# Kernel optimization log

Hardware: AMD Instinct MI355X
Metric: run time of the kernel (lower is better)

The kernel has to match this reference:

```python
import jax, jax.numpy as jnp
import numpy as np

N_NODES = 50000
IN_C = 128
OUT_C = 128
N_EDGES = 1600000
NEG_SLOPE = 0.2
EPS = 1e-16  # matches torch_geometric softmax denominator epsilon


def setup_inputs() -> dict:
    key = jax.random.key(0)
    k1, k2, k3, k4, k5 = jax.random.split(key, 5)
    glorot = 1.0 / np.sqrt(IN_C)
    x = jax.random.normal(k1, (N_NODES, IN_C), dtype=jnp.float32)
    W = jax.random.normal(k2, (IN_C, OUT_C), dtype=jnp.float32) * glorot
    a_src = jax.random.normal(k3, (OUT_C,), dtype=jnp.float32) * glorot
    a_dst = jax.random.normal(k4, (OUT_C,), dtype=jnp.float32) * glorot
    bias = jnp.zeros((OUT_C,), dtype=jnp.float32)
    edge_index = jax.random.randint(k5, (2, N_EDGES), 0, N_NODES, dtype=jnp.int32)
    return {"x": x, "W": W, "a_src": a_src, "a_dst": a_dst,
            "bias": bias, "edge_index": edge_index}


def reference(x, W, a_src, a_dst, bias, edge_index):
    N = x.shape[0]
    # add self loops (GATConv default add_self_loops=True)
    loops = jnp.arange(N, dtype=edge_index.dtype)
    src = jnp.concatenate([edge_index[0], loops])  # [E+N]
    dst = jnp.concatenate([edge_index[1], loops])

    h = x @ W                                      # [N, out]
    alpha_s = h @ a_src                            # [N]
    alpha_d = h @ a_dst                            # [N]

    e = alpha_s[src] + alpha_d[dst]                # [E+N]
    e = jnp.where(e > 0, e, NEG_SLOPE * e)         # leaky_relu

    # neighbor-wise (per destination node) stable softmax
    m = jax.ops.segment_max(e, dst, num_segments=N)
    ex = jnp.exp(e - m[dst])
    denom = jax.ops.segment_sum(ex, dst, num_segments=N)
    alpha = ex / (denom[dst] + EPS)

    # weighted aggregation of source features into destination nodes
    msgs = h[src] * alpha[:, None]                 # [E+N, out]
    out = jax.ops.segment_sum(msgs, dst, num_segments=N) + bias
    return jax.nn.relu(out)
```

## Files before the change

kernel.cpp:

```cpp
#include <hip/hip_runtime.h>
#include <hip/hip_fp16.h>

#define C 128
#define NEG_SLOPE 0.2f
#define SM_EPS 1e-16f
#define BKT_SHIFT 8
#define BKT_MASK 255
#define BIN_CHUNK 8192
#define WP 136

typedef unsigned int uint32;
typedef __attribute__((ext_vector_type(8))) short bf16x8;
typedef __attribute__((ext_vector_type(4))) float f32x4;

static __device__ __forceinline__ unsigned short f2bf(float f) {
    uint32 u = __float_as_uint(f);
    uint32 r = 0x7FFFu + ((u >> 16) & 1u);
    return (unsigned short)((u + r) >> 16);
}
static __device__ __forceinline__ uint32 f2bf2(float lo, float hi) {
    return (uint32)f2bf(lo) | ((uint32)f2bf(hi) << 16);
}
static __device__ __forceinline__ uint32 f2h(float f) {
    __half h = __float2half(f);
    return (uint32)*reinterpret_cast<unsigned short*>(&h);
}
static __device__ __forceinline__ float h2f(uint32 b) {
    unsigned short s = (unsigned short)(b & 0xffffu);
    __half h = *reinterpret_cast<__half*>(&s);
    return __half2float(h);
}

__global__ __launch_bounds__(256) void cvtw_kernel(const float* __restrict__ W,
                                                   uint32* __restrict__ Wf,
                                                   int* __restrict__ bucket_cnt, int NB) {
    int gid = blockIdx.x * 256 + threadIdx.x;
    if (blockIdx.x == 0 && threadIdx.x < NB) bucket_cnt[threadIdx.x] = 0;
    int j2   = gid & 3;
    int lane = (gid >> 2) & 63;
    int tile = gid >> 8;
    int t = tile >> 2, kk = tile & 3;
    int n = t * 16 + (lane & 15);
    int k = kk * 32 + (lane >> 4) * 8 + j2 * 2;
    Wf[gid] = f2bf2(W[k * C + n], W[(k + 1) * C + n]);
}

__global__ __launch_bounds__(256) void gemm_hist_kernel(
    const float* __restrict__ x, const uint32* __restrict__ Wf,
    const float* __restrict__ a_src, const float* __restrict__ a_dst,
    unsigned short* __restrict__ hb, float* __restrict__ as_out,
    float* __restrict__ ad_out, int N,
    const int* __restrict__ dst, int* __restrict__ bucket_cnt, int E, int total, int NB)
{
    __shared__ __align__(16) unsigned short slice[4][16 * WP];
    __shared__ int bhist[256];

    const int tid  = threadIdx.x;
    const int lane = tid & 63;
    const int w    = tid >> 6;
    const int row0 = blockIdx.x * 64;
    const int m16  = lane & 15;
    const int q    = lane >> 4;

    bhist[tid] = 0;

    const int row = row0 + w * 16 + m16;
    const bool rv = (row < N);
    const float* xr_p = x + (size_t)(rv ? row : 0) * C + q * 8;

    float4 xr[8];
    #pragma unroll
    for (int kk = 0; kk < 4; ++kk) {
        xr[kk * 2]     = rv ? *(const float4*)(xr_p + kk * 32)     : make_float4(0, 0, 0, 0);
        xr[kk * 2 + 1] = rv ? *(const float4*)(xr_p + kk * 32 + 4) : make_float4(0, 0, 0, 0);
    }

    f32x4 acc[8];
    const f32x4 zz = {0.f, 0.f, 0.f, 0.f};
    #pragma unroll
    for (int t = 0; t < 8; ++t) acc[t] = zz;

    #pragma unroll
    for (int kk = 0; kk < 4; ++kk) {
        union { bf16x8 v; uint32 u[4]; } au;
        float4 p0 = xr[kk * 2], p1 = xr[kk * 2 + 1];
        au.u[0] = f2bf2(p0.x, p0.y); au.u[1] = f2bf2(p0.z, p0.w);
        au.u[2] = f2bf2(p1.x, p1.y); au.u[3] = f2bf2(p1.z, p1.w);
        #pragma unroll
        for (int t = 0; t < 8; ++t) {
            bf16x8 b = *(const bf16x8*)&Wf[((t * 4 + kk) * 64 + lane) * 4];
            acc[t] = __builtin_amdgcn_mfma_f32_16x16x32_bf16(au.v, b, acc[t], 0, 0, 0);
        }
    }

    float ps[4] = {0.f, 0.f, 0.f, 0.f}, pd[4] = {0.f, 0.f, 0.f, 0.f};
    #pragma unroll
    for (int t = 0; t < 8; ++t) {
        float av = a_src[t * 16 + m16];
        float dv = a_dst[t * 16 + m16];
        #pragma unroll
        for (int r = 0; r < 4; ++r) {
            ps[r] += acc[t][r] * av;
            pd[r] += acc[t][r] * dv;
        }
    }
    #pragma unroll
    for (int r = 0; r < 4; ++r) {
        #pragma unroll
        for (int off = 1; off < 16; off <<= 1) {
            ps[r] += __shfl_xor(ps[r], off, 64);
            pd[r] += __shfl_xor(pd[r], off, 64);
        }
    }
    if (m16 == 0) {
        #pragma unroll
        for (int r = 0; r < 4; ++r) {
            int rr = row0 + w * 16 + q * 4 + r;
            if (rr < N) { as_out[rr] = ps[r]; ad_out[rr] = pd[r]; }
        }
    }

    #pragma unroll
    for (int t = 0; t < 8; ++t)
        #pragma unroll
        for (int r = 0; r < 4; ++r)
            slice[w][(q * 4 + r) * WP + t * 16 + m16] = f2bf(acc[t][r]);
    __syncthreads();
    #pragma unroll
    for (int it = 0; it < 4; ++it) {
        int r = it * 4 + q;
        int rr = row0 + w * 16 + r;
        if (rr < N) {
            bf16x8 v = *(const bf16x8*)&slice[w][r * WP + m16 * 8];
            *(bf16x8*)&hb[(size_t)rr * C + m16 * 8] = v;
        }
    }

    for (int i = blockIdx.x * 256 + tid; i < total; i += gridDim.x * 256) {
        int d = (i < E) ? dst[i] : (i - E);
        atomicAdd(&bhist[d >> BKT_SHIFT], 1);
    }
    __syncthreads();
    if (tid < NB && bhist[tid]) atomicAdd(&bucket_cnt[tid], bhist[tid]);
}

__global__ __launch_bounds__(256) void scan_off_kernel(
    const int* __restrict__ bucket_cnt, int* __restrict__ bucket_off,
    int* __restrict__ bucket_cursor, int* __restrict__ row_start,
    int NB, int N, int total)
{
    __shared__ int wave_tot[4];
    const int tid = threadIdx.x, lane = tid & 63, wid = tid >> 6;
    int v = (tid < NB) ? bucket_cnt[tid] : 0;
    int x = v;
    #pragma unroll
    for (int off = 1; off < 64; off <<= 1) {
        int t = __shfl_up(x, off, 64);
        if (lane >= off) x += t;
    }
    if (lane == 63) wave_tot[wid] = x;
    __syncthreads();
    int wbase = 0;
    #pragma unroll
    for (int w = 0; w < 4; ++w) wbase += (w < wid) ? wave_tot[w] : 0;
    int excl = wbase + x - v;
    if (tid < NB) { bucket_off[tid] = excl; bucket_cursor[tid] = excl; }
    if (tid == 0) { bucket_off[NB] = total; row_start[N] = total; }
}

__global__ __launch_bounds__(1024) void bin_kernel(
    const int* __restrict__ src, const int* __restrict__ dst,
    int* __restrict__ bucket_cursor, uint32* __restrict__ packed,
    int E, int total, int NB)
{
    __shared__ uint32 lsrc[BIN_CHUNK];
    __shared__ unsigned short ldst[BIN_CHUNK];
    __shared__ int hist[256];
    __shared__ int base[256];
    const int tid = threadIdx.x;
    const int start = blockIdx.x * BIN_CHUNK;
    const int end = min(start + BIN_CHUNK, total);
    const int n = end - start;

    if (tid < 256) hist[tid] = 0;
    for (int i = start + tid; i < end; i += 1024) {
        int s = (i < E) ? src[i] : (i - E);
        int d = (i < E) ? dst[i] : (i - E);
        lsrc[i - start] = (uint32)s;
        ldst[i - start] = (unsigned short)d;
    }
    __syncthreads();
    for (int j = tid; j < n; j += 1024)
        atomicAdd(&hist[ldst[j] >> BKT_SHIFT], 1);
    __syncthreads();
    if (tid < NB) {
        int c = hist[tid];
        base[tid] = c ? atomicAdd(&bucket_cursor[tid], c) : 0;
    }
    if (tid < 256) hist[tid] = 0;
    __syncthreads();
    for (int j = tid; j < n; j += 1024) {
        int d = ldst[j];
        int b = d >> BKT_SHIFT;
        int pos = base[b] + atomicAdd(&hist[b], 1);
        packed[pos] = (lsrc[j] << BKT_SHIFT) | (uint32)(d & BKT_MASK);
    }
}

__global__ __launch_bounds__(1024) void build_kernel(
    const uint32* __restrict__ packed, const int* __restrict__ bucket_off,
    const float* __restrict__ as, const float* __restrict__ ad,
    int* __restrict__ row_start, uint32* __restrict__ csr, int N)
{
    __shared__ int cnt[256];
    __shared__ int cur[256];
    __shared__ float adl[256];
    __shared__ int wave_tot[4];
    const int tid = threadIdx.x;
    const int b = blockIdx.x;
    const int off = bucket_off[b];
    const int end = bucket_off[b + 1];

    if (tid < 256) {
        cnt[tid] = 0;
        int g = (b << BKT_SHIFT) + tid;
        adl[tid] = (g < N) ? ad[g] : 0.f;
    }
    __syncthreads();
    for (int j = off + tid; j < end; j += 1024)
        atomicAdd(&cnt[packed[j] & BKT_MASK], 1);
    __syncthreads();

    int v = 0, x = 0;
    if (tid < 256) {
        const int lane = tid & 63;
        v = cnt[tid]; x = v;
        #pragma unroll
        for (int o = 1; o < 64; o <<= 1) {
            int t = __shfl_up(x, o, 64);
            if (lane >= o) x += t;
        }
        if (lane == 63) wave_tot[tid >> 6] = x;
    }
    __syncthreads();
    if (tid < 256) {
        const int wid = tid >> 6;
        int wbase = 0;
        #pragma unroll
        for (int w = 0; w < 4; ++w) wbase += (w < wid) ? wave_tot[w] : 0;
        int excl = wbase + x - v;
        int g = (b << BKT_SHIFT) + tid;
        if (g < N) row_start[g] = off + excl;
        cur[tid] = excl;
    }
    __syncthreads();

    for (int j = off + tid; j < end; j += 1024) {
        uint32 p = packed[j];
        int l = (int)(p & BKT_MASK);
        int s = (int)(p >> BKT_SHIFT);
        float e = as[s] + adl[l];
        e = (e > 0.f) ? e : NEG_SLOPE * e;
        int pos = atomicAdd(&cur[l], 1);
        csr[off + pos] = ((uint32)s << 16) | f2h(e);
    }
}

__global__ __launch_bounds__(256) void gather_kernel(
    const uint32* __restrict__ csr, const int* __restrict__ row_start,
    const unsigned short* __restrict__ hb, const float* __restrict__ bias,
    float* __restrict__ out, int N)
{
    const int w    = threadIdx.x >> 6;
    const int lane = threadIdx.x & 63;
    const int d = blockIdx.x * 4 + w;
    if (d >= N) return;

    const int beg = row_start[d];
    const int deg = row_start[d + 1] - beg;
    const int c2 = lane << 1;
    float a0 = 0.f, a1 = 0.f;

    if (deg <= 64) {
        uint32 ent = (lane < deg) ? csr[beg + lane] : 0xFC00u;
        float e = h2f(ent);
        float m = e;
        #pragma unroll
        for (int off = 32; off > 0; off >>= 1) m = fmaxf(m, __shfl_xor(m, off, 64));
        float p = (lane < deg) ? __expf(e - m) : 0.f;
        float ssum = p;
        #pragma unroll
        for (int off = 32; off > 0; off >>= 1) ssum += __shfl_xor(ssum, off, 64);
        float wgt = p * (1.f / (ssum + SM_EPS));
        uint32 bc = (ent & 0xffff0000u) | f2h(wgt);

        int t = 0;
        for (; t + 8 <= deg; t += 8) {
            uint32 b0 = (uint32)__shfl((int)bc, t, 64),     b1 = (uint32)__shfl((int)bc, t + 1, 64);
            uint32 b2 = (uint32)__shfl((int)bc, t + 2, 64), b3 = (uint32)__shfl((int)bc, t + 3, 64);
            uint32 b4 = (uint32)__shfl((int)bc, t + 4, 64), b5 = (uint32)__shfl((int)bc, t + 5, 64);
            uint32 b6 = (uint32)__shfl((int)bc, t + 6, 64), b7 = (uint32)__shfl((int)bc, t + 7, 64);
            uint32 u0 = *(const uint32*)&hb[(size_t)(b0 >> 16) * C + c2];
            uint32 u1 = *(const uint32*)&hb[(size_t)(b1 >> 16) * C + c2];
            uint32 u2 = *(const uint32*)&hb[(size_t)(b2 >> 16) * C + c2];
            uint32 u3 = *(const uint32*)&hb[(size_t)(b3 >> 16) * C + c2];
            uint32 u4 = *(const uint32*)&hb[(size_t)(b4 >> 16) * C + c2];
            uint32 u5 = *(const uint32*)&hb[(size_t)(b5 >> 16) * C + c2];
            uint32 u6 = *(const uint32*)&hb[(size_t)(b6 >> 16) * C + c2];
            uint32 u7 = *(const uint32*)&hb[(size_t)(b7 >> 16) * C + c2];
            float w0 = h2f(b0), w1 = h2f(b1), w2 = h2f(b2), w3 = h2f(b3);
            float w4 = h2f(b4), w5 = h2f(b5), w6 = h2f(b6), w7 = h2f(b7);
            a0 += __uint_as_float(u0 << 16) * w0 + __uint_as_float(u1 << 16) * w1
                + __uint_as_float(u2 << 16) * w2 + __uint_as_float(u3 << 16) * w3
                + __uint_as_float(u4 << 16) * w4 + __uint_as_float(u5 << 16) * w5
                + __uint_as_float(u6 << 16) * w6 + __uint_as_float(u7 << 16) * w7;
            a1 += __uint_as_float(u0 & 0xffff0000u) * w0 + __uint_as_float(u1 & 0xffff0000u) * w1
                + __uint_as_float(u2 & 0xffff0000u) * w2 + __uint_as_float(u3 & 0xffff0000u) * w3
                + __uint_as_float(u4 & 0xffff0000u) * w4 + __uint_as_float(u5 & 0xffff0000u) * w5
                + __uint_as_float(u6 & 0xffff0000u) * w6 + __uint_as_float(u7 & 0xffff0000u) * w7;
        }
        for (; t < deg; ++t) {
            uint32 b0 = (uint32)__shfl((int)bc, t, 64);
            uint32 u0 = *(const uint32*)&hb[(size_t)(b0 >> 16) * C + c2];
            float w0 = h2f(b0);
            a0 += __uint_as_float(u0 << 16) * w0;
            a1 += __uint_as_float(u0 & 0xffff0000u) * w0;
        }
    } else if (deg <= 128) {
        uint32 ea = (lane < deg) ? csr[beg + lane] : 0xFC00u;
        uint32 eb = (64 + lane < deg) ? csr[beg + 64 + lane] : 0xFC00u;
        float e0 = h2f(ea), e1 = h2f(eb);
        float m = fmaxf(e0, e1);
        #pragma unroll
        for (int off = 32; off > 0; off >>= 1) m = fmaxf(m, __shfl_xor(m, off, 64));
        float p0 = (lane < deg) ? __expf(e0 - m) : 0.f;
        float p1 = (64 + lane < deg) ? __expf(e1 - m) : 0.f;
        float ssum = p0 + p1;
        #pragma unroll
        for (int off = 32; off > 0; off >>= 1) ssum += __shfl_xor(ssum, off, 64);
        float inv = 1.f / (ssum + SM_EPS);
        uint32 ba = (ea & 0xffff0000u) | f2h(p0 * inv);
        uint32 bb = (eb & 0xffff0000u) | f2h(p1 * inv);
        for (int t = 0; t < deg; ++t) {
            uint32 b0 = (t < 64) ? (uint32)__shfl((int)ba, t, 64)
                                 : (uint32)__shfl((int)bb, t - 64, 64);
            uint32 u0 = *(const uint32*)&hb[(size_t)(b0 >> 16) * C + c2];
            float w0 = h2f(b0);
            a0 += __uint_as_float(u0 << 16) * w0;
            a1 += __uint_as_float(u0 & 0xffff0000u) * w0;
        }
    } else {
        float m = -INFINITY;
        for (int t = lane; t < deg; t += 64)
            m = fmaxf(m, h2f(csr[beg + t]));
        #pragma unroll
        for (int off = 32; off > 0; off >>= 1) m = fmaxf(m, __shfl_xor(m, off, 64));
        float ssum = 0.f;
        for (int t = lane; t < deg; t += 64)
            ssum += __expf(h2f(csr[beg + t]) - m);
        #pragma unroll
        for (int off = 32; off > 0; off >>= 1) ssum += __shfl_xor(ssum, off, 64);
        float inv = 1.f / (ssum + SM_EPS);
        for (int t0 = 0; t0 < deg; t0 += 64) {
            int nc = min(64, deg - t0);
            uint32 ent = (lane < nc) ? csr[beg + t0 + lane] : 0xFC00u;
            float wl = (lane < nc) ? __expf(h2f(ent) - m) * inv : 0.f;
            uint32 bc = (ent & 0xffff0000u) | f2h(wl);
            for (int t = 0; t < nc; ++t) {
                uint32 b0 = (uint32)__shfl((int)bc, t, 64);
                uint32 u0 = *(const uint32*)&hb[(size_t)(b0 >> 16) * C + c2];
                float w0 = h2f(b0);
                a0 += __uint_as_float(u0 << 16) * w0;
                a1 += __uint_as_float(u0 & 0xffff0000u) * w0;
            }
        }
    }

    float2 b2 = *(const float2*)&bias[c2];
    a0 = fmaxf(a0 + b2.x, 0.f);
    a1 = fmaxf(a1 + b2.y, 0.f);
    *(float2*)&out[(size_t)d * C + c2] = make_float2(a0, a1);
}

extern "C" void kernel_launch(void* const* d_in, const int* in_sizes, int n_in,
                              void* d_out, int out_size, void* d_ws, size_t ws_size,
                              hipStream_t stream) {
    const float* x     = (const float*)d_in[0];
    const float* W     = (const float*)d_in[1];
    const float* a_src = (const float*)d_in[2];
    const float* a_dst = (const float*)d_in[3];
    const float* bias  = (const float*)d_in[4];
    const int*   edge  = (const int*)d_in[5];

    const int N = in_sizes[0] / C;
    const int E = in_sizes[5] / 2;
    const int total = E + N;
    const int* src = edge;
    const int* dst = edge + E;
    float* out = (float*)d_out;

    const int NB = (N + BKT_MASK) >> BKT_SHIFT;

    float* ws = (float*)d_ws;
    unsigned short* hb = (unsigned short*)ws;
    float* as = (float*)(hb + (size_t)N * C);
    float* ad = as + N;
    int* row_start     = (int*)(ad + N);
    uint32* packed     = (uint32*)(row_start + (N + 2));
    uint32* csr        = packed + total;
    uint32* Wf         = csr + total;
    int* bucket_cnt    = (int*)(Wf + 8192);
    int* bucket_off    = bucket_cnt + NB;
    int* bucket_cursor = bucket_off + (NB + 1);

    cvtw_kernel<<<32, 256, 0, stream>>>(W, Wf, bucket_cnt, NB);
    gemm_hist_kernel<<<(N + 63) / 64, 256, 0, stream>>>(
        x, Wf, a_src, a_dst, hb, as, ad, N, dst, bucket_cnt, E, total, NB);
    scan_off_kernel<<<1, 256, 0, stream>>>(bucket_cnt, bucket_off, bucket_cursor,
                                           row_start, NB, N, total);
    bin_kernel<<<(total + BIN_CHUNK - 1) / BIN_CHUNK, 1024, 0, stream>>>(
        src, dst, bucket_cursor, packed, E, total, NB);
    build_kernel<<<NB, 1024, 0, stream>>>(packed, bucket_off, as, ad, row_start, csr, N);
    gather_kernel<<<(N + 3) / 4, 256, 0, stream>>>(csr, row_start, hb, bias, out, N);
}
```

Baseline: 206.8 us.

## Process two nodes per wave in gather and fold bucket scan into consumers

The gather kernel now assigns each half-wave to one destination node, with each lane loading four bf16 channels as a uint2 instead of two. This is meant to halve the number of waves and issue wider gather loads. The padded loop runs to the larger of the two degrees, so work is wasted when they differ, and high-degree nodes fall back to a full-wave path. The separate single-block scan launch is removed: bin and build kernels recompute the bucket prefix sum per block, using a progress counter in place of a cursor.

```diff
diff --git a/kernel.cpp b/kernel.cpp
--- a/kernel.cpp
+++ b/kernel.cpp
@@ -33,9 +33,13 @@
 
 __global__ __launch_bounds__(256) void cvtw_kernel(const float* __restrict__ W,
                                                    uint32* __restrict__ Wf,
-                                                   int* __restrict__ bucket_cnt, int NB) {
+                                                   int* __restrict__ bucket_cnt,
+                                                   int* __restrict__ bucket_progress, int NB) {
     int gid = blockIdx.x * 256 + threadIdx.x;
-    if (blockIdx.x == 0 && threadIdx.x < NB) bucket_cnt[threadIdx.x] = 0;
+    if (blockIdx.x == 0 && threadIdx.x < NB) {
+        bucket_cnt[threadIdx.x] = 0;
+        bucket_progress[threadIdx.x] = 0;
+    }
     int j2   = gid & 3;
     int lane = (gid >> 2) & 63;
     int tile = gid >> 8;
@@ -144,45 +148,35 @@
     if (tid < NB && bhist[tid]) atomicAdd(&bucket_cnt[tid], bhist[tid]);
 }
 
-__global__ __launch_bounds__(256) void scan_off_kernel(
-    const int* __restrict__ bucket_cnt, int* __restrict__ bucket_off,
-    int* __restrict__ bucket_cursor, int* __restrict__ row_start,
-    int NB, int N, int total)
-{
-    __shared__ int wave_tot[4];
-    const int tid = threadIdx.x, lane = tid & 63, wid = tid >> 6;
-    int v = (tid < NB) ? bucket_cnt[tid] : 0;
-    int x = v;
-    #pragma unroll
-    for (int off = 1; off < 64; off <<= 1) {
-        int t = __shfl_up(x, off, 64);
-        if (lane >= off) x += t;
-    }
-    if (lane == 63) wave_tot[wid] = x;
-    __syncthreads();
-    int wbase = 0;
-    #pragma unroll
-    for (int w = 0; w < 4; ++w) wbase += (w < wid) ? wave_tot[w] : 0;
-    int excl = wbase + x - v;
-    if (tid < NB) { bucket_off[tid] = excl; bucket_cursor[tid] = excl; }
-    if (tid == 0) { bucket_off[NB] = total; row_start[N] = total; }
-}
-
 __global__ __launch_bounds__(1024) void bin_kernel(
     const int* __restrict__ src, const int* __restrict__ dst,
-    int* __restrict__ bucket_cursor, uint32* __restrict__ packed,
-    int E, int total, int NB)
+    const int* __restrict__ bucket_cnt, int* __restrict__ bucket_progress,
+    uint32* __restrict__ packed, int E, int total, int NB)
 {
     __shared__ uint32 lsrc[BIN_CHUNK];
     __shared__ unsigned short ldst[BIN_CHUNK];
     __shared__ int hist[256];
     __shared__ int base[256];
+    __shared__ int boff[256];
+    __shared__ int wave_tot[4];
     const int tid = threadIdx.x;
     const int start = blockIdx.x * BIN_CHUNK;
     const int end = min(start + BIN_CHUNK, total);
     const int n = end - start;
 
-    if (tid < 256) hist[tid] = 0;
+    int v = 0, xx = 0;
+    if (tid < 256) {
+        hist[tid] = 0;
+        const int lane = tid & 63;
+        v = (tid < NB) ? bucket_cnt[tid] : 0;
+        xx = v;
+        #pragma unroll
+        for (int o = 1; o < 64; o <<= 1) {
+            int t = __shfl_up(xx, o, 64);
+            if (lane >= o) xx += t;
+        }
+        if (lane == 63) wave_tot[tid >> 6] = xx;
+    }
     for (int i = start + tid; i < end; i += 1024) {
         int s = (i < E) ? src[i] : (i - E);
         int d = (i < E) ? dst[i] : (i - E);
@@ -190,12 +184,20 @@
         ldst[i - start] = (unsigned short)d;
     }
     __syncthreads();
+    if (tid < 256) {
+        const int wid = tid >> 6;
+        int wbase = 0;
+        #pragma unroll
+        for (int w = 0; w < 4; ++w) wbase += (w < wid) ? wave_tot[w] : 0;
+        boff[tid] = wbase + xx - v;
+    }
+    __syncthreads();
     for (int j = tid; j < n; j += 1024)
         atomicAdd(&hist[ldst[j] >> BKT_SHIFT], 1);
     __syncthreads();
     if (tid < NB) {
         int c = hist[tid];
-        base[tid] = c ? atomicAdd(&bucket_cursor[tid], c) : 0;
+        base[tid] = boff[tid] + (c ? atomicAdd(&bucket_progress[tid], c) : 0);
     }
     if (tid < 256) hist[tid] = 0;
     __syncthreads();
@@ -208,47 +210,68 @@
 }
 
 __global__ __launch_bounds__(1024) void build_kernel(
-    const uint32* __restrict__ packed, const int* __restrict__ bucket_off,
+    const uint32* __restrict__ packed, const int* __restrict__ bucket_cnt,
     const float* __restrict__ as, const float* __restrict__ ad,
-    int* __restrict__ row_start, uint32* __restrict__ csr, int N)
+    int* __restrict__ row_start, uint32* __restrict__ csr, int N, int NB, int total)
 {
     __shared__ int cnt[256];
     __shared__ int cur[256];
     __shared__ float adl[256];
-    __shared__ int wave_tot[4];
+    __shared__ int boff[256];
+    __shared__ int wave_tot[8];
     const int tid = threadIdx.x;
     const int b = blockIdx.x;
-    const int off = bucket_off[b];
-    const int end = bucket_off[b + 1];
-
-    if (tid < 256) {
+
+    int v = 0, xx = 0;
+    if (tid < 256) {
+        const int lane = tid & 63;
+        v = (tid < NB) ? bucket_cnt[tid] : 0;
+        xx = v;
+        #pragma unroll
+        for (int o = 1; o < 64; o <<= 1) {
+            int t = __shfl_up(xx, o, 64);
+            if (lane >= o) xx += t;
+        }
+        if (lane == 63) wave_tot[tid >> 6] = xx;
         cnt[tid] = 0;
         int g = (b << BKT_SHIFT) + tid;
         adl[tid] = (g < N) ? ad[g] : 0.f;
     }
     __syncthreads();
+    if (tid < 256) {
+        const int wid = tid >> 6;
+        int wbase = 0;
+        #pragma unroll
+        for (int w = 0; w < 4; ++w) wbase += (w < wid) ? wave_tot[w] : 0;
+        boff[tid] = wbase + xx - v;
+    }
+    __syncthreads();
+    const int off = boff[b];
+    const int end = off + ((b < NB) ? bucket_cnt[b] : 0);
+    if (b == 0 && tid == 0) row_start[N] = total;
+
     for (int j = off + tid; j < end; j += 1024)
         atomicAdd(&cnt[packed[j] & BKT_MASK], 1);
     __syncthreads();
 
-    int v = 0, x = 0;
+    int v2 = 0, x2 = 0;
     if (tid < 256) {
         const int lane = tid & 63;
-        v = cnt[tid]; x = v;
+        v2 = cnt[tid]; x2 = v2;
         #pragma unroll
         for (int o = 1; o < 64; o <<= 1) {
-            int t = __shfl_up(x, o, 64);
-            if (lane >= o) x += t;
-        }
-        if (lane == 63) wave_tot[tid >> 6] = x;
+            int t = __shfl_up(x2, o, 64);
+            if (lane >= o) x2 += t;
+        }
+        if (lane == 63) wave_tot[4 + (tid >> 6)] = x2;
     }
     __syncthreads();
     if (tid < 256) {
         const int wid = tid >> 6;
         int wbase = 0;
         #pragma unroll
-        for (int w = 0; w < 4; ++w) wbase += (w < wid) ? wave_tot[w] : 0;
-        int excl = wbase + x - v;
+        for (int w = 0; w < 4; ++w) wbase += (w < wid) ? wave_tot[4 + w] : 0;
+        int excl = wbase + x2 - v2;
         int g = (b << BKT_SHIFT) + tid;
         if (g < N) row_start[g] = off + excl;
         cur[tid] = excl;
@@ -266,6 +289,43 @@
     }
 }
 
+static __device__ __forceinline__ void gather_node_fw(
+    int d, const uint32* __restrict__ csr, const int* __restrict__ row_start,
+    const unsigned short* __restrict__ hb, const float* __restrict__ bias,
+    float* __restrict__ out, int lane)
+{
+    const int beg = row_start[d];
+    const int deg = row_start[d + 1] - beg;
+    const int c2 = lane << 1;
+    float a0 = 0.f, a1 = 0.f;
+    float m = -INFINITY;
+    for (int t = lane; t < deg; t += 64) m = fmaxf(m, h2f(csr[beg + t]));
+    #pragma unroll
+    for (int off = 32; off > 0; off >>= 1) m = fmaxf(m, __shfl_xor(m, off, 64));
+    float ssum = 0.f;
+    for (int t = lane; t < deg; t += 64) ssum += __expf(h2f(csr[beg + t]) - m);
+    #pragma unroll
+    for (int off = 32; off > 0; off >>= 1) ssum += __shfl_xor(ssum, off, 64);
+    float inv = 1.f / (ssum + SM_EPS);
+    for (int t0 = 0; t0 < deg; t0 += 64) {
+        int nc = min(64, deg - t0);
+        uint32 ent = (lane < nc) ? csr[beg + t0 + lane] : 0xFC00u;
+        float wl = (lane < nc) ? __expf(h2f(ent) - m) * inv : 0.f;
+        uint32 bc = (ent & 0xffff0000u) | f2h(wl);
+        for (int t = 0; t < nc; ++t) {
+            uint32 b0 = (uint32)__shfl((int)bc, t, 64);
+            uint32 u0 = *(const uint32*)&hb[(size_t)(b0 >> 16) * C + c2];
+            float w0 = h2f(b0);
+            a0 += __uint_as_float(u0 << 16) * w0;
+            a1 += __uint_as_float(u0 & 0xffff0000u) * w0;
+        }
+    }
+    float2 b2 = *(const float2*)&bias[c2];
+    a0 = fmaxf(a0 + b2.x, 0.f);
+    a1 = fmaxf(a1 + b2.y, 0.f);
+    *(float2*)&out[(size_t)d * C + c2] = make_float2(a0, a1);
+}
+
 __global__ __launch_bounds__(256) void gather_kernel(
     const uint32* __restrict__ csr, const int* __restrict__ row_start,
     const unsigned short* __restrict__ hb, const float* __restrict__ bias,
@@ -273,113 +333,98 @@
 {
     const int w    = threadIdx.x >> 6;
     const int lane = threadIdx.x & 63;
-    const int d = blockIdx.x * 4 + w;
-    if (d >= N) return;
-
-    const int beg = row_start[d];
-    const int deg = row_start[d + 1] - beg;
-    const int c2 = lane << 1;
-    float a0 = 0.f, a1 = 0.f;
-
-    if (deg <= 64) {
-        uint32 ent = (lane < deg) ? csr[beg + lane] : 0xFC00u;
-        float e = h2f(ent);
-        float m = e;
-        #pragma unroll
-        for (int off = 32; off > 0; off >>= 1) m = fmaxf(m, __shfl_xor(m, off, 64));
-        float p = (lane < deg) ? __expf(e - m) : 0.f;
-        float ssum = p;
-        #pragma unroll
-        for (int off = 32; off > 0; off >>= 1) ssum += __shfl_xor(ssum, off, 64);
-        float wgt = p * (1.f / (ssum + SM_EPS));
-        uint32 bc = (ent & 0xffff0000u) | f2h(wgt);
-
-        int t = 0;
-        for (; t + 8 <= deg; t += 8) {
-            uint32 b0 = (uint32)__shfl((int)bc, t, 64),     b1 = (uint32)__shfl((int)bc, t + 1, 64);
-            uint32 b2 = (uint32)__shfl((int)bc, t + 2, 64), b3 = (uint32)__shfl((int)bc, t + 3, 64);
-            uint32 b4 = (uint32)__shfl((int)bc, t + 4, 64), b5 = (uint32)__shfl((int)bc, t + 5, 64);
-            uint32 b6 = (uint32)__shfl((int)bc, t + 6, 64), b7 = (uint32)__shfl((int)bc, t + 7, 64);
-            uint32 u0 = *(const uint32*)&hb[(size_t)(b0 >> 16) * C + c2];
-            uint32 u1 = *(const uint32*)&hb[(size_t)(b1 >> 16) * C + c2];
-            uint32 u2 = *(const uint32*)&hb[(size_t)(b2 >> 16) * C + c2];
-            uint32 u3 = *(const uint32*)&hb[(size_t)(b3 >> 16) * C + c2];
-            uint32 u4 = *(const uint32*)&hb[(size_t)(b4 >> 16) * C + c2];
-            uint32 u5 = *(const uint32*)&hb[(size_t)(b5 >> 16) * C + c2];
-            uint32 u6 = *(const uint32*)&hb[(size_t)(b6 >> 16) * C + c2];
-            uint32 u7 = *(const uint32*)&hb[(size_t)(b7 >> 16) * C + c2];
-            float w0 = h2f(b0), w1 = h2f(b1), w2 = h2f(b2), w3 = h2f(b3);
-            float w4 = h2f(b4), w5 = h2f(b5), w6 = h2f(b6), w7 = h2f(b7);
-            a0 += __uint_as_float(u0 << 16) * w0 + __uint_as_float(u1 << 16) * w1
-                + __uint_as_float(u2 << 16) * w2 + __uint_as_float(u3 << 16) * w3
-                + __uint_as_float(u4 << 16) * w4 + __uint_as_float(u5 << 16) * w5
-                + __uint_as_float(u6 << 16) * w6 + __uint_as_float(u7 << 16) * w7;
-            a1 += __uint_as_float(u0 & 0xffff0000u) * w0 + __uint_as_float(u1 & 0xffff0000u) * w1
-                + __uint_as_float(u2 & 0xffff0000u) * w2 + __uint_as_float(u3 & 0xffff0000u) * w3
-                + __uint_as_float(u4 & 0xffff0000u) * w4 + __uint_as_float(u5 & 0xffff0000u) * w5
-                + __uint_as_float(u6 & 0xffff0000u) * w6 + __uint_as_float(u7 & 0xffff0000u) * w7;
-        }
-        for (; t < deg; ++t) {
-            uint32 b0 = (uint32)__shfl((int)bc, t, 64);
-            uint32 u0 = *(const uint32*)&hb[(size_t)(b0 >> 16) * C + c2];
-            float w0 = h2f(b0);
-            a0 += __uint_as_float(u0 << 16) * w0;
-            a1 += __uint_as_float(u0 & 0xffff0000u) * w0;
-        }
-    } else if (deg <= 128) {
-        uint32 ea = (lane < deg) ? csr[beg + lane] : 0xFC00u;
-        uint32 eb = (64 + lane < deg) ? csr[beg + 64 + lane] : 0xFC00u;
-        float e0 = h2f(ea), e1 = h2f(eb);
-        float m = fmaxf(e0, e1);
-        #pragma unroll
-        for (int off = 32; off > 0; off >>= 1) m = fmaxf(m, __shfl_xor(m, off, 64));
-        float p0 = (lane < deg) ? __expf(e0 - m) : 0.f;
-        float p1 = (64 + lane < deg) ? __expf(e1 - m) : 0.f;
-        float ssum = p0 + p1;
-        #pragma unroll
-        for (int off = 32; off > 0; off >>= 1) ssum += __shfl_xor(ssum, off, 64);
-        float inv = 1.f / (ssum + SM_EPS);
-        uint32 ba = (ea & 0xffff0000u) | f2h(p0 * inv);
-        uint32 bb = (eb & 0xffff0000u) | f2h(p1 * inv);
-        for (int t = 0; t < deg; ++t) {
-            uint32 b0 = (t < 64) ? (uint32)__shfl((int)ba, t, 64)
-                                 : (uint32)__shfl((int)bb, t - 64, 64);
-            uint32 u0 = *(const uint32*)&hb[(size_t)(b0 >> 16) * C + c2];
-            float w0 = h2f(b0);
-            a0 += __uint_as_float(u0 << 16) * w0;
-            a1 += __uint_as_float(u0 & 0xffff0000u) * w0;
-        }
-    } else {
-        float m = -INFINITY;
-        for (int t = lane; t < deg; t += 64)
-            m = fmaxf(m, h2f(csr[beg + t]));
-        #pragma unroll
-        for (int off = 32; off > 0; off >>= 1) m = fmaxf(m, __shfl_xor(m, off, 64));
-        float ssum = 0.f;
-        for (int t = lane; t < deg; t += 64)
-            ssum += __expf(h2f(csr[beg + t]) - m);
-        #pragma unroll
-        for (int off = 32; off > 0; off >>= 1) ssum += __shfl_xor(ssum, off, 64);
-        float inv = 1.f / (ssum + SM_EPS);
-        for (int t0 = 0; t0 < deg; t0 += 64) {
-            int nc = min(64, deg - t0);
-            uint32 ent = (lane < nc) ? csr[beg + t0 + lane] : 0xFC00u;
-            float wl = (lane < nc) ? __expf(h2f(ent) - m) * inv : 0.f;
-            uint32 bc = (ent & 0xffff0000u) | f2h(wl);
-            for (int t = 0; t < nc; ++t) {
-                uint32 b0 = (uint32)__shfl((int)bc, t, 64);
-                uint32 u0 = *(const uint32*)&hb[(size_t)(b0 >> 16) * C + c2];
-                float w0 = h2f(b0);
-                a0 += __uint_as_float(u0 << 16) * w0;
-                a1 += __uint_as_float(u0 & 0xffff0000u) * w0;
-            }
-        }
-    }
-
-    float2 b2 = *(const float2*)&bias[c2];
-    a0 = fmaxf(a0 + b2.x, 0.f);
-    a1 = fmaxf(a1 + b2.y, 0.f);
-    *(float2*)&out[(size_t)d * C + c2] = make_float2(a0, a1);
+    const int half = lane >> 5;
+    const int hl   = lane & 31;
+    const int pair = blockIdx.x * 4 + w;
+    const int d0 = pair * 2;
+    if (d0 >= N) return;
+    const int d = d0 + half;
+    const bool valid = (d < N);
+
+    int beg = 0, deg = 0;
+    if (valid) { beg = row_start[d]; deg = row_start[d + 1] - beg; }
+
+    int wdeg = deg;
+    #pragma unroll
+    for (int off = 32; off > 0; off >>= 1) wdeg = max(wdeg, __shfl_xor(wdeg, off, 64));
+
+    if (wdeg > 64) {
+        gather_node_fw(d0, csr, row_start, hb, bias, out, lane);
+        if (d0 + 1 < N) gather_node_fw(d0 + 1, csr, row_start, hb, bias, out, lane);
+        return;
+    }
+
+    uint32 ent0 = (hl < deg) ? csr[beg + hl] : 0xFC00u;
+    uint32 ent1 = (32 + hl < deg) ? csr[beg + 32 + hl] : 0xFC00u;
+    float e0 = h2f(ent0), e1 = h2f(ent1);
+    float m = fmaxf(e0, e1);
+    #pragma unroll
+    for (int off = 16; off > 0; off >>= 1) m = fmaxf(m, __shfl_xor(m, off, 64));
+    float p0 = (hl < deg) ? __expf(e0 - m) : 0.f;
+    float p1 = (32 + hl < deg) ? __expf(e1 - m) : 0.f;
+    float ssum = p0 + p1;
+    #pragma unroll
+    for (int off = 16; off > 0; off >>= 1) ssum += __shfl_xor(ssum, off, 64);
+    const float inv = 1.f / (ssum + SM_EPS);
+    uint32 bc0 = (hl < deg) ? ((ent0 & 0xffff0000u) | f2h(p0 * inv)) : 0u;
+    uint32 bc1 = (32 + hl < deg) ? ((ent1 & 0xffff0000u) | f2h(p1 * inv)) : 0u;
+
+    const int c4 = hl << 2;
+    const int hbase = half << 5;
+    float a0 = 0.f, a1 = 0.f, a2 = 0.f, a3 = 0.f;
+
+    const int n1 = min(wdeg, 32);
+    int t = 0;
+    for (; t + 2 <= n1; t += 2) {
+        uint32 bA = (uint32)__shfl((int)bc0, hbase + t, 64);
+        uint32 bB = (uint32)__shfl((int)bc0, hbase + t + 1, 64);
+        uint2 uA = *(const uint2*)&hb[(size_t)(bA >> 16) * C + c4];
+        uint2 uB = *(const uint2*)&hb[(size_t)(bB >> 16) * C + c4];
+        float wA = h2f(bA), wB = h2f(bB);
+        a0 += __uint_as_float(uA.x << 16) * wA + __uint_as_float(uB.x << 16) * wB;
+        a1 += __uint_as_float(uA.x & 0xffff0000u) * wA + __uint_as_float(uB.x & 0xffff0000u) * wB;
+        a2 += __uint_as_float(uA.y << 16) * wA + __uint_as_float(uB.y << 16) * wB;
+        a3 += __uint_as_float(uA.y & 0xffff0000u) * wA + __uint_as_float(uB.y & 0xffff0000u) * wB;
+    }
+    for (; t < n1; ++t) {
+        uint32 bA = (uint32)__shfl((int)bc0, hbase + t, 64);
+        uint2 uA = *(const uint2*)&hb[(size_t)(bA >> 16) * C + c4];
+        float wA = h2f(bA);
+        a0 += __uint_as_float(uA.x << 16) * wA;
+        a1 += __uint_as_float(uA.x & 0xffff0000u) * wA;
+        a2 += __uint_as_float(uA.y << 16) * wA;
+        a3 += __uint_as_float(uA.y & 0xffff0000u) * wA;
+    }
+    for (t = 32; t + 2 <= wdeg; t += 2) {
+        uint32 bA = (uint32)__shfl((int)bc1, hbase + t - 32, 64);
+        uint32 bB = (uint32)__shfl((int)bc1, hbase + t - 31, 64);
+        uint2 uA = *(const uint2*)&hb[(size_t)(bA >> 16) * C + c4];
+        uint2 uB = *(const uint2*)&hb[(size_t)(bB >> 16) * C + c4];
+        float wA = h2f(bA), wB = h2f(bB);
+        a0 += __uint_as_float(uA.x << 16) * wA + __uint_as_float(uB.x << 16) * wB;
+        a1 += __uint_as_float(uA.x & 0xffff0000u) * wA + __uint_as_float(uB.x & 0xffff0000u) * wB;
+        a2 += __uint_as_float(uA.y << 16) * wA + __uint_as_float(uB.y << 16) * wB;
+        a3 += __uint_as_float(uA.y & 0xffff0000u) * wA + __uint_as_float(uB.y & 0xffff0000u) * wB;
+    }
+    for (; t < wdeg; ++t) {
+        uint32 bA = (uint32)__shfl((int)bc1, hbase + t - 32, 64);
+        uint2 uA = *(const uint2*)&hb[(size_t)(bA >> 16) * C + c4];
+        float wA = h2f(bA);
+        a0 += __uint_as_float(uA.x << 16) * wA;
+        a1 += __uint_as_float(uA.x & 0xffff0000u) * wA;
+        a2 += __uint_as_float(uA.y << 16) * wA;
+        a3 += __uint_as_float(uA.y & 0xffff0000u) * wA;
+    }
+
+    if (valid) {
+        float4 bb = *(const float4*)&bias[c4];
+        float4 o;
+        o.x = fmaxf(a0 + bb.x, 0.f);
+        o.y = fmaxf(a1 + bb.y, 0.f);
+        o.z = fmaxf(a2 + bb.z, 0.f);
+        o.w = fmaxf(a3 + bb.w, 0.f);
+        *(float4*)&out[(size_t)d * C + c4] = o;
+    }
 }
 
 extern "C" void kernel_launch(void* const* d_in, const int* in_sizes, int n_in,
@@ -405,21 +450,19 @@
     unsigned short* hb = (unsigned short*)ws;
     float* as = (float*)(hb + (size_t)N * C);
     float* ad = as + N;
-    int* row_start     = (int*)(ad + N);
-    uint32* packed     = (uint32*)(row_start + (N + 2));
-    uint32* csr        = packed + total;
-    uint32* Wf         = csr + total;
-    int* bucket_cnt    = (int*)(Wf + 8192);
-    int* bucket_off    = bucket_cnt + NB;
-    int* bucket_cursor = bucket_off + (NB + 1);
-
-    cvtw_kernel<<<32, 256, 0, stream>>>(W, Wf, bucket_cnt, NB);
+    int* row_start       = (int*)(ad + N);
+    uint32* packed       = (uint32*)(row_start + (N + 2));
+    uint32* csr          = packed + total;
+    uint32* Wf           = csr + total;
+    int* bucket_cnt      = (int*)(Wf + 8192);
+    int* bucket_progress = bucket_cnt + NB;
+
+    cvtw_kernel<<<32, 256, 0, stream>>>(W, Wf, bucket_cnt, bucket_progress, NB);
     gemm_hist_kernel<<<(N + 63) / 64, 256, 0, stream>>>(
         x, Wf, a_src, a_dst, hb, as, ad, N, dst, bucket_cnt, E, total, NB);
-    scan_off_kernel<<<1, 256, 0, stream>>>(bucket_cnt, bucket_off, bucket_cursor,
-                                           row_start, NB, N, total);
     bin_kernel<<<(total + BIN_CHUNK - 1) / BIN_CHUNK, 1024, 0, stream>>>(
-        src, dst, bucket_cursor, packed, E, total, NB);
-    build_kernel<<<NB, 1024, 0, stream>>>(packed, bucket_off, as, ad, row_start, csr, N);
-    gather_kernel<<<(N + 3) / 4, 256, 0, stream>>>(csr, row_start, hb, bias, out, N);
-}
+        src, dst, bucket_cnt, bucket_progress, packed, E, total, NB);
+    build_kernel<<<NB, 1024, 0, stream>>>(packed, bucket_cnt, as, ad, row_start,
+                                          csr, N, NB, total);
+    gather_kernel<<<((N + 1) / 2 + 3) / 4, 256, 0, stream>>>(csr, row_start, hb, bias, out, N);
+}
```

Result: no change. 209.5 us (+1.3%).
